# Kernel optimization log

Measured on AMD Instinct MI355X. Metric: run time of the kernel, lower is better.

Reference implementation:

```python
import jax, jax.numpy as jnp
import numpy as np

D = 4096
B = 8192
LN_EPS = 1e-5


def setup_inputs() -> dict:
    key = jax.random.key(0)
    k1, k2, k3 = jax.random.split(key, 3)
    x = jax.random.normal(k1, (B, D), dtype=jnp.float32)
    x0 = jax.random.normal(k2, (B, D), dtype=jnp.float32)
    # xavier_normal_ on (D, 1): std = sqrt(2 / (D + 1))
    weight = jax.random.normal(k3, (D,), dtype=jnp.float32) * np.float32(np.sqrt(2.0 / (D + 1)))
    bias = jnp.zeros((D,), dtype=jnp.float32)
    gamma = jnp.ones((D,), dtype=jnp.float32)   # LayerNorm weight
    beta = jnp.zeros((D,), dtype=jnp.float32)   # LayerNorm bias
    return {"x": x, "x0": x0, "weight": weight, "bias": bias, "gamma": gamma, "beta": beta}


def reference(x, x0, weight, bias, gamma, beta):
    # torch: (x[:,:,None] @ x0[:,None,:]) @ weight  ==  x * (x0 @ weight)
    # weighted[b,i] = sum_j x[b,i] * x0[b,j] * w[j] = x[b,i] * (x0[b] . w)
    scale = x0 @ weight                      # (B,)  per-batch scalar
    pre = x * scale[:, None] + bias + x      # scale + bias + residual, (B, D)
    # LayerNorm over last dim
    mean = jnp.mean(pre, axis=-1, keepdims=True)
    var = jnp.mean(jnp.square(pre - mean), axis=-1, keepdims=True)
    out = (pre - mean) * jax.lax.rsqrt(var + LN_EPS) * gamma + beta
    # dropout is identity at inference
    return out
```

## Files before the change

kernel.cpp:

```cpp
#include <hip/hip_runtime.h>

#define DIM 4096
#define LN_EPS 1e-5f
#define NTHREADS 256
#define VEC_PER_THREAD 4

typedef float vfloat4 __attribute__((ext_vector_type(4)));

__global__ __launch_bounds__(NTHREADS) void crosslayer_ln_kernel(
    const float* __restrict__ x,
    const float* __restrict__ x0,
    const float* __restrict__ w,
    const float* __restrict__ bias,
    const float* __restrict__ gamma,
    const float* __restrict__ beta,
    float* __restrict__ out)
{
    const int row = blockIdx.x;
    const int tid = threadIdx.x;
    const int wave = tid >> 6;
    const int lane = tid & 63;

    const float4* __restrict__ x0v = reinterpret_cast<const float4*>(x0 + (size_t)row * DIM);
    const float4* __restrict__ xv  = reinterpret_cast<const float4*>(x  + (size_t)row * DIM);
    const float4* __restrict__ wv  = reinterpret_cast<const float4*>(w);
    const float4* __restrict__ bv  = reinterpret_cast<const float4*>(bias);
    const float4* __restrict__ gv  = reinterpret_cast<const float4*>(gamma);
    const float4* __restrict__ btv = reinterpret_cast<const float4*>(beta);
    vfloat4* __restrict__ ov = reinterpret_cast<vfloat4*>(out + (size_t)row * DIM);

    float4 xr[VEC_PER_THREAD];
    float dot = 0.f;
    #pragma unroll
    for (int p = 0; p < VEC_PER_THREAD; ++p) {
        const int idx = p * NTHREADS + tid;
        const float4 a = x0v[idx];
        const float4 b = wv[idx];
        xr[p] = xv[idx];
        dot += a.x * b.x + a.y * b.y + a.z * b.z + a.w * b.w;
    }
    #pragma unroll
    for (int o = 1; o < 64; o <<= 1) dot += __shfl_xor(dot, o, 64);

    __shared__ float sdot[4];
    if (lane == 0) sdot[wave] = dot;
    __syncthreads();
    const float s = sdot[0] + sdot[1] + sdot[2] + sdot[3];
    const float m = 1.f + s;

    float4 pre[VEC_PER_THREAD];
    float sum = 0.f, sumsq = 0.f;
    #pragma unroll
    for (int p = 0; p < VEC_PER_THREAD; ++p) {
        const int idx = p * NTHREADS + tid;
        const float4 b = bv[idx];
        float4 pv;
        pv.x = fmaf(xr[p].x, m, b.x);
        pv.y = fmaf(xr[p].y, m, b.y);
        pv.z = fmaf(xr[p].z, m, b.z);
        pv.w = fmaf(xr[p].w, m, b.w);
        pre[p] = pv;
        sum   += pv.x + pv.y + pv.z + pv.w;
        sumsq += pv.x * pv.x + pv.y * pv.y + pv.z * pv.z + pv.w * pv.w;
    }
    #pragma unroll
    for (int o = 1; o < 64; o <<= 1) {
        sum   += __shfl_xor(sum,   o, 64);
        sumsq += __shfl_xor(sumsq, o, 64);
    }
    __shared__ float ssum[4], ssq[4];
    if (lane == 0) { ssum[wave] = sum; ssq[wave] = sumsq; }
    __syncthreads();
    const float tsum = ssum[0] + ssum[1] + ssum[2] + ssum[3];
    const float tsq  = ssq[0]  + ssq[1]  + ssq[2]  + ssq[3];
    const float mean = tsum * (1.f / DIM);
    const float var  = tsq * (1.f / DIM) - mean * mean;
    const float inv  = rsqrtf(var + LN_EPS);

    #pragma unroll
    for (int p = 0; p < VEC_PER_THREAD; ++p) {
        const int idx = p * NTHREADS + tid;
        const float4 g  = gv[idx];
        const float4 bt = btv[idx];
        vfloat4 o;
        o.x = fmaf((pre[p].x - mean) * inv, g.x, bt.x);
        o.y = fmaf((pre[p].y - mean) * inv, g.y, bt.y);
        o.z = fmaf((pre[p].z - mean) * inv, g.z, bt.z);
        o.w = fmaf((pre[p].w - mean) * inv, g.w, bt.w);
        __builtin_nontemporal_store(o, &ov[idx]);
    }
}

extern "C" void kernel_launch(void* const* d_in, const int* in_sizes, int n_in,
                              void* d_out, int out_size, void* d_ws, size_t ws_size,
                              hipStream_t stream) {
    const float* x     = (const float*)d_in[0];
    const float* x0    = (const float*)d_in[1];
    const float* w     = (const float*)d_in[2];
    const float* bias  = (const float*)d_in[3];
    const float* gamma = (const float*)d_in[4];
    const float* beta  = (const float*)d_in[5];
    float* out = (float*)d_out;

    const int B = in_sizes[0] / DIM;
    crosslayer_ln_kernel<<<B, NTHREADS, 0, stream>>>(x, x0, w, bias, gamma, beta, out);
}
```

Before: 61.49 us.

## Fuse dot and LayerNorm statistics into one reduction using algebraic moment expansion

Computes the mean and variance of the pre-norm values algebraically from per-row sums of x, x², x·b, b and b² together with the dot product. This lets all six quantities be reduced in a single shuffle and shared-memory pass, dropping one block-wide barrier. The block size also goes from 256 to 512 threads with two float4 per thread, and the gamma/beta loads are issued before the reduction. In exchange it runs more shuffles and relies on the E[x²]-mean² expansion in terms of m, which can lose float precision for large scale factors.

```diff
diff --git a/kernel.cpp b/kernel.cpp
--- a/kernel.cpp
+++ b/kernel.cpp
@@ -2,8 +2,9 @@
 
 #define DIM 4096
 #define LN_EPS 1e-5f
-#define NTHREADS 256
-#define VEC_PER_THREAD 4
+#define NTHREADS 512
+#define VPT 2
+#define NWAVES (NTHREADS / 64)
 
 typedef float vfloat4 __attribute__((ext_vector_type(4)));
 
@@ -29,66 +30,75 @@
     const float4* __restrict__ btv = reinterpret_cast<const float4*>(beta);
     vfloat4* __restrict__ ov = reinterpret_cast<vfloat4*>(out + (size_t)row * DIM);
 
-    float4 xr[VEC_PER_THREAD];
-    float dot = 0.f;
-    #pragma unroll
-    for (int p = 0; p < VEC_PER_THREAD; ++p) {
-        const int idx = p * NTHREADS + tid;
-        const float4 a = x0v[idx];
-        const float4 b = wv[idx];
-        xr[p] = xv[idx];
-        dot += a.x * b.x + a.y * b.y + a.z * b.z + a.w * b.w;
-    }
-    #pragma unroll
-    for (int o = 1; o < 64; o <<= 1) dot += __shfl_xor(dot, o, 64);
+    const int i0 = tid;
+    const int i1 = NTHREADS + tid;
 
-    __shared__ float sdot[4];
-    if (lane == 0) sdot[wave] = dot;
-    __syncthreads();
-    const float s = sdot[0] + sdot[1] + sdot[2] + sdot[3];
-    const float m = 1.f + s;
+    const float4 a0 = x0v[i0];
+    const float4 a1 = x0v[i1];
+    const float4 w0 = wv[i0];
+    const float4 w1 = wv[i1];
+    const float4 xA = xv[i0];
+    const float4 xB = xv[i1];
+    const float4 bA = bv[i0];
+    const float4 bB = bv[i1];
 
-    float4 pre[VEC_PER_THREAD];
-    float sum = 0.f, sumsq = 0.f;
-    #pragma unroll
-    for (int p = 0; p < VEC_PER_THREAD; ++p) {
-        const int idx = p * NTHREADS + tid;
-        const float4 b = bv[idx];
-        float4 pv;
-        pv.x = fmaf(xr[p].x, m, b.x);
-        pv.y = fmaf(xr[p].y, m, b.y);
-        pv.z = fmaf(xr[p].z, m, b.z);
-        pv.w = fmaf(xr[p].w, m, b.w);
-        pre[p] = pv;
-        sum   += pv.x + pv.y + pv.z + pv.w;
-        sumsq += pv.x * pv.x + pv.y * pv.y + pv.z * pv.z + pv.w * pv.w;
-    }
+    float dot = a0.x*w0.x + a0.y*w0.y + a0.z*w0.z + a0.w*w0.w
+              + a1.x*w1.x + a1.y*w1.y + a1.z*w1.z + a1.w*w1.w;
+    float Sx  = xA.x + xA.y + xA.z + xA.w + xB.x + xB.y + xB.z + xB.w;
+    float Sxx = xA.x*xA.x + xA.y*xA.y + xA.z*xA.z + xA.w*xA.w
+              + xB.x*xB.x + xB.y*xB.y + xB.z*xB.z + xB.w*xB.w;
+    float Sxb = xA.x*bA.x + xA.y*bA.y + xA.z*bA.z + xA.w*bA.w
+              + xB.x*bB.x + xB.y*bB.y + xB.z*bB.z + xB.w*bB.w;
+    float Sb  = bA.x + bA.y + bA.z + bA.w + bB.x + bB.y + bB.z + bB.w;
+    float Sbb = bA.x*bA.x + bA.y*bA.y + bA.z*bA.z + bA.w*bA.w
+              + bB.x*bB.x + bB.y*bB.y + bB.z*bB.z + bB.w*bB.w;
+
+    const float4 gA  = gv[i0];
+    const float4 gB  = gv[i1];
+    const float4 btA = btv[i0];
+    const float4 btB = btv[i1];
+
     #pragma unroll
     for (int o = 1; o < 64; o <<= 1) {
-        sum   += __shfl_xor(sum,   o, 64);
-        sumsq += __shfl_xor(sumsq, o, 64);
+        dot += __shfl_xor(dot, o, 64);
+        Sx  += __shfl_xor(Sx,  o, 64);
+        Sxx += __shfl_xor(Sxx, o, 64);
+        Sxb += __shfl_xor(Sxb, o, 64);
+        Sb  += __shfl_xor(Sb,  o, 64);
+        Sbb += __shfl_xor(Sbb, o, 64);
     }
-    __shared__ float ssum[4], ssq[4];
-    if (lane == 0) { ssum[wave] = sum; ssq[wave] = sumsq; }
+
+    __shared__ float red[6][NWAVES];
+    if (lane == 0) {
+        red[0][wave] = dot; red[1][wave] = Sx;  red[2][wave] = Sxx;
+        red[3][wave] = Sxb; red[4][wave] = Sb;  red[5][wave] = Sbb;
+    }
     __syncthreads();
-    const float tsum = ssum[0] + ssum[1] + ssum[2] + ssum[3];
-    const float tsq  = ssq[0]  + ssq[1]  + ssq[2]  + ssq[3];
-    const float mean = tsum * (1.f / DIM);
-    const float var  = tsq * (1.f / DIM) - mean * mean;
+
+    float tdot = 0.f, tSx = 0.f, tSxx = 0.f, tSxb = 0.f, tSb = 0.f, tSbb = 0.f;
+    #pragma unroll
+    for (int i = 0; i < NWAVES; ++i) {
+        tdot += red[0][i]; tSx  += red[1][i]; tSxx += red[2][i];
+        tSxb += red[3][i]; tSb  += red[4][i]; tSbb += red[5][i];
+    }
+
+    const float m    = 1.f + tdot;
+    const float mean = (m * tSx + tSb) * (1.f / DIM);
+    const float Ex2  = (m * m * tSxx + 2.f * m * tSxb + tSbb) * (1.f / DIM);
+    const float var  = Ex2 - mean * mean;
     const float inv  = rsqrtf(var + LN_EPS);
 
-    #pragma unroll
-    for (int p = 0; p < VEC_PER_THREAD; ++p) {
-        const int idx = p * NTHREADS + tid;
-        const float4 g  = gv[idx];
-        const float4 bt = btv[idx];
-        vfloat4 o;
-        o.x = fmaf((pre[p].x - mean) * inv, g.x, bt.x);
-        o.y = fmaf((pre[p].y - mean) * inv, g.y, bt.y);
-        o.z = fmaf((pre[p].z - mean) * inv, g.z, bt.z);
-        o.w = fmaf((pre[p].w - mean) * inv, g.w, bt.w);
-        __builtin_nontemporal_store(o, &ov[idx]);
-    }
+    vfloat4 o0, o1;
+    o0.x = fmaf((fmaf(m, xA.x, bA.x) - mean) * inv, gA.x, btA.x);
+    o0.y = fmaf((fmaf(m, xA.y, bA.y) - mean) * inv, gA.y, btA.y);
+    o0.z = fmaf((fmaf(m, xA.z, bA.z) - mean) * inv, gA.z, btA.z);
+    o0.w = fmaf((fmaf(m, xA.w, bA.w) - mean) * inv, gA.w, btA.w);
+    o1.x = fmaf((fmaf(m, xB.x, bB.x) - mean) * inv, gB.x, btB.x);
+    o1.y = fmaf((fmaf(m, xB.y, bB.y) - mean) * inv, gB.y, btB.y);
+    o1.z = fmaf((fmaf(m, xB.z, bB.z) - mean) * inv, gB.z, btB.z);
+    o1.w = fmaf((fmaf(m, xB.w, bB.w) - mean) * inv, gB.w, btB.w);
+    __builtin_nontemporal_store(o0, &ov[i0]);
+    __builtin_nontemporal_store(o1, &ov[i1]);
 }
 
 extern "C" void kernel_launch(void* const* d_in, const int* in_sizes, int n_in,
```

Result: slower. 63.61 us (+3.4%).
